# Optimization experiments

Measured on AMD Instinct MI355X. Metric: run time of the kernel, lower is better.

The kernel has to match this reference:

```python
import jax, jax.numpy as jnp
import numpy as np

FIX_SIGMA = (1.0, 2.0, 4.0, 8.0, 16.0)


def setup_inputs() -> dict:
    key = jax.random.key(0)
    k1, k2 = jax.random.split(key)
    B, C, D = 512, 32, 512
    source = jax.random.normal(k1, (B, C, D), dtype=jnp.float32)
    target = jax.random.normal(k2, (B, C, D), dtype=jnp.float32)
    return {"source": source, "target": target}


def _mmd(source, target):
    B = source.shape[0]
    total = jnp.concatenate([source, target], axis=0)  # [N, C, D], N = 2B
    # Pairwise per-channel squared L2 distance via norm expansion
    # (mathematically identical to ((x_i - x_j)**2).sum(-1), no [N,N,C,D] intermediate)
    sq = jnp.sum(total * total, axis=-1)  # [N, C]
    cross = jnp.einsum("icd,jcd->ijc", total, total)  # [N, N, C]
    L2 = sq[:, None, :] + sq[None, :, :] - 2.0 * cross  # [N, N, C]
    kernels = sum(jnp.exp(-L2 / sigma) for sigma in FIX_SIGMA)  # [N, N, C]
    XX = kernels[:B, :B, :]
    YY = kernels[B:, B:, :]
    XY = kernels[:B, B:, :]
    YX = kernels[B:, :B, :]
    loss_1 = XX + YY - XY - YX  # [B, B, C]
    # mean over dim0, mean over dim0 again (i.e. both batch dims), sum over channels
    return jnp.sum(jnp.mean(loss_1, axis=(0, 1)))


def reference(source, target):
    return _mmd(source, target)
```

## Files before the change

kernel.cpp:

```cpp
#include <hip/hip_runtime.h>

namespace {

constexpr int kC = 32;
constexpr int kD = 512;
constexpr int kB = 512;
constexpr int kN = 1024;
constexpr int kCD = kC * kD;
constexpr int BM = 128;
constexpr int BK = 64;
constexpr int KSTEPS = kD / BK;
constexpr int TILES = kN / BM;
constexpr int NPAIRS = TILES * (TILES + 1) / 2;

typedef float f32x4 __attribute__((ext_vector_type(4)));
typedef short s16x8 __attribute__((ext_vector_type(8)));

__device__ inline unsigned int pack_bf16(float a, float b) {
  unsigned int ua = __float_as_uint(a);
  unsigned int ub = __float_as_uint(b);
  ua += 0x7fffu + ((ua >> 16) & 1u);
  ub += 0x7fffu + ((ub >> 16) & 1u);
  return (ua >> 16) | (ub & 0xffff0000u);
}

__global__ void prep_kernel(const float* __restrict__ src,
                            const float* __restrict__ tgt,
                            float* __restrict__ sq,
                            unsigned int* __restrict__ tot) {
  int gw = (blockIdx.x * blockDim.x + threadIdx.x) >> 6;
  int lane = threadIdx.x & 63;
  int i = gw >> 5;
  int c = gw & 31;
  const float* p = (i < kB ? src + (size_t)i * kCD
                           : tgt + (size_t)(i - kB) * kCD) + c * kD;
  f32x4 v0 = *(const f32x4*)(p + lane * 8);
  f32x4 v1 = *(const f32x4*)(p + lane * 8 + 4);

  uint4 w = make_uint4(pack_bf16(v0.x, v0.y), pack_bf16(v0.z, v0.w),
                       pack_bf16(v1.x, v1.y), pack_bf16(v1.z, v1.w));
  *(uint4*)(tot + (size_t)(c * kN + i) * (kD / 2) + lane * 4) = w;

  float s = v0.x * v0.x + v0.y * v0.y + v0.z * v0.z + v0.w * v0.w
          + v1.x * v1.x + v1.y * v1.y + v1.z * v1.z + v1.w * v1.w;
#pragma unroll
  for (int o = 32; o > 0; o >>= 1) s += __shfl_down(s, o);
  if (lane == 0) sq[c * kN + i] = s;
}

__launch_bounds__(256, 2)
__global__ void mmd_kernel(const unsigned short* __restrict__ tot,
                           const float* __restrict__ sq,
                           float* __restrict__ out) {
  int b = blockIdx.x;
  int c = b & 31;
  int p = b >> 5;
  int ti = 0;
  while (p >= TILES - ti) { p -= TILES - ti; ++ti; }
  int tj = ti + p;

  __shared__ __align__(16) unsigned short lA[2][BM * BK];
  __shared__ __align__(16) unsigned short lB[2][BM * BK];
  __shared__ float wsum[4];

  const int t = threadIdx.x;
  const int lane = t & 63;
  const int wid = t >> 6;
  const int wr = wid >> 1;
  const int wc = wid & 1;

  const unsigned short* gA = tot + (size_t)(c * kN + ti * BM) * kD;
  const unsigned short* gB = tot + (size_t)(c * kN + tj * BM) * kD;

  const int srow = lane >> 3;
  const int sslot = lane & 7;

  auto STAGE = [&](int buf, int ks) {
#pragma unroll
    for (int q = 0; q < 4; ++q) {
      int row = (q * 4 + wid) * 8 + srow;
      int chunk = sslot ^ (row & 7);
      const unsigned short* sa = gA + (size_t)row * kD + ks * BK + chunk * 8;
      const unsigned short* sb = gB + (size_t)row * kD + ks * BK + chunk * 8;
      __builtin_amdgcn_global_load_lds(
          (const __attribute__((address_space(1))) unsigned int*)sa,
          (__attribute__((address_space(3))) unsigned int*)&lA[buf][(q * 4 + wid) * 512],
          16, 0, 0);
      __builtin_amdgcn_global_load_lds(
          (const __attribute__((address_space(1))) unsigned int*)sb,
          (__attribute__((address_space(3))) unsigned int*)&lB[buf][(q * 4 + wid) * 512],
          16, 0, 0);
    }
  };

  f32x4 acc[4][4] = {};

  STAGE(0, 0);
  __syncthreads();

  int cur = 0;
  for (int ks = 0; ks < KSTEPS; ++ks) {
    if (ks + 1 < KSTEPS) STAGE(cur ^ 1, ks + 1);

    const s16x8* A8 = (const s16x8*)lA[cur];
    const s16x8* B8 = (const s16x8*)lB[cur];
#pragma unroll
    for (int kk = 0; kk < 2; ++kk) {
      s16x8 aF[4], bF[4];
#pragma unroll
      for (int m = 0; m < 4; ++m) {
        int row = wr * 64 + m * 16 + (lane & 15);
        aF[m] = A8[row * 8 + ((kk * 4 + (lane >> 4)) ^ (row & 7))];
      }
#pragma unroll
      for (int n = 0; n < 4; ++n) {
        int row = wc * 64 + n * 16 + (lane & 15);
        bF[n] = B8[row * 8 + ((kk * 4 + (lane >> 4)) ^ (row & 7))];
      }
#pragma unroll
      for (int m = 0; m < 4; ++m)
#pragma unroll
        for (int n = 0; n < 4; ++n)
          acc[m][n] = __builtin_amdgcn_mfma_f32_16x16x32_bf16(
              aF[m], bF[n], acc[m][n], 0, 0, 0);
    }

    __syncthreads();
    cur ^= 1;
  }

  const float sA = (ti < TILES / 2) ? 1.f : -1.f;
  const float sB = (tj < TILES / 2) ? 1.f : -1.f;
  const float scale = sA * sB * ((ti == tj) ? 1.f : 2.f) / 262144.f;
  const float* sqA = sq + c * kN + ti * BM;
  const float* sqB = sq + c * kN + tj * BM;

  float local = 0.f;
#pragma unroll
  for (int m = 0; m < 4; ++m) {
    float sqa_r[4];
#pragma unroll
    for (int rI = 0; rI < 4; ++rI)
      sqa_r[rI] = sqA[wr * 64 + m * 16 + (lane >> 4) * 4 + rI];
#pragma unroll
    for (int n = 0; n < 4; ++n) {
      float sqb_ = sqB[wc * 64 + n * 16 + (lane & 15)];
#pragma unroll
      for (int rI = 0; rI < 4; ++rI) {
        float L2 = sqa_r[rI] + sqb_ - 2.f * acc[m][n][rI];
        float tt = __expf(L2 * -0.0625f);
        float t2 = tt * tt, t4 = t2 * t2, t8 = t4 * t4;
        local += tt + t2 + t4 + t8 + t8 * t8;
      }
    }
  }

#pragma unroll
  for (int o = 32; o > 0; o >>= 1) local += __shfl_down(local, o);
  if (lane == 0) wsum[wid] = local;
  __syncthreads();
  if (t == 0)
    atomicAdd(out, (wsum[0] + wsum[1] + wsum[2] + wsum[3]) * scale);
}

}

extern "C" void kernel_launch(void* const* d_in, const int* in_sizes, int n_in,
                              void* d_out, int out_size, void* d_ws,
                              size_t ws_size, hipStream_t stream) {
  const float* src = (const float*)d_in[0];
  const float* tgt = (const float*)d_in[1];
  float* out = (float*)d_out;

  float* sq = (float*)d_ws;
  unsigned int* tot = (unsigned int*)((char*)d_ws + (size_t)kC * kN * 4);

  (void)hipMemsetAsync(d_out, 0, sizeof(float), stream);

  {
    int blocks = (kN * kC) / 4;
    prep_kernel<<<blocks, 256, 0, stream>>>(src, tgt, sq, tot);
  }
  {
    mmd_kernel<<<NPAIRS * kC, 256, 0, stream>>>((const unsigned short*)tot, sq, out);
  }
}
```

Measured before the change: 59.92 us.

## Halve K tile, new LDS swizzle layout, raise occupancy, fold memset into prep

Shrinks the K-step tile from 64 to 32, which halves LDS use per block, and raises the launch bound to 4 waves-per-SIMD occupancy. It replaces the row-XOR swizzle with a new paired-row layout and precomputed per-lane LDS offsets, so fragment reads need one pointer plus constant offsets. The output zeroing moves from a separate memset into the prep kernel, removing one launch. The cost is twice as many k-steps and barriers, plus a tighter register budget that could cause spills.

```diff
diff --git a/kernel.cpp b/kernel.cpp
--- a/kernel.cpp
+++ b/kernel.cpp
@@ -8,7 +8,7 @@
 constexpr int kN = 1024;
 constexpr int kCD = kC * kD;
 constexpr int BM = 128;
-constexpr int BK = 64;
+constexpr int BK = 32;
 constexpr int KSTEPS = kD / BK;
 constexpr int TILES = kN / BM;
 constexpr int NPAIRS = TILES * (TILES + 1) / 2;
@@ -27,7 +27,9 @@
 __global__ void prep_kernel(const float* __restrict__ src,
                             const float* __restrict__ tgt,
                             float* __restrict__ sq,
-                            unsigned int* __restrict__ tot) {
+                            unsigned int* __restrict__ tot,
+                            float* __restrict__ out) {
+  if (blockIdx.x == 0 && threadIdx.x == 0) *out = 0.f;
   int gw = (blockIdx.x * blockDim.x + threadIdx.x) >> 6;
   int lane = threadIdx.x & 63;
   int i = gw >> 5;
@@ -48,7 +50,7 @@
   if (lane == 0) sq[c * kN + i] = s;
 }
 
-__launch_bounds__(256, 2)
+__launch_bounds__(256, 4)
 __global__ void mmd_kernel(const unsigned short* __restrict__ tot,
                            const float* __restrict__ sq,
                            float* __restrict__ out) {
@@ -72,26 +74,31 @@
   const unsigned short* gA = tot + (size_t)(c * kN + ti * BM) * kD;
   const unsigned short* gB = tot + (size_t)(c * kN + tj * BM) * kD;
 
-  const int srow = lane >> 3;
-  const int sslot = lane & 7;
+  const int srow = ((lane >> 3) << 1) + ((lane >> 2) & 1);
+  const int scch = (lane & 3) ^ ((lane >> 3) & 3);
 
   auto STAGE = [&](int buf, int ks) {
 #pragma unroll
-    for (int q = 0; q < 4; ++q) {
-      int row = (q * 4 + wid) * 8 + srow;
-      int chunk = sslot ^ (row & 7);
-      const unsigned short* sa = gA + (size_t)row * kD + ks * BK + chunk * 8;
-      const unsigned short* sb = gB + (size_t)row * kD + ks * BK + chunk * 8;
+    for (int q = 0; q < 2; ++q) {
+      int i = wid * 2 + q;
+      int r = 16 * i + srow;
+      const unsigned short* sa = gA + (size_t)r * kD + ks * BK + scch * 8;
+      const unsigned short* sb = gB + (size_t)r * kD + ks * BK + scch * 8;
       __builtin_amdgcn_global_load_lds(
           (const __attribute__((address_space(1))) unsigned int*)sa,
-          (__attribute__((address_space(3))) unsigned int*)&lA[buf][(q * 4 + wid) * 512],
+          (__attribute__((address_space(3))) unsigned int*)&lA[buf][i * 512],
           16, 0, 0);
       __builtin_amdgcn_global_load_lds(
           (const __attribute__((address_space(1))) unsigned int*)sb,
-          (__attribute__((address_space(3))) unsigned int*)&lB[buf][(q * 4 + wid) * 512],
+          (__attribute__((address_space(3))) unsigned int*)&lB[buf][i * 512],
           16, 0, 0);
     }
   };
+
+  const int l15 = lane & 15;
+  const int s4 = lane >> 4;
+  const int laneoff = ((l15 >> 1) << 7) + ((l15 & 1) << 6) +
+                      ((s4 ^ ((l15 >> 1) & 3)) << 4);
 
   f32x4 acc[4][4] = {};
 
@@ -102,28 +109,19 @@
   for (int ks = 0; ks < KSTEPS; ++ks) {
     if (ks + 1 < KSTEPS) STAGE(cur ^ 1, ks + 1);
 
-    const s16x8* A8 = (const s16x8*)lA[cur];
-    const s16x8* B8 = (const s16x8*)lB[cur];
+    const char* Abase = (const char*)lA[cur] + wr * 4096 + laneoff;
+    const char* Bbase = (const char*)lB[cur] + wc * 4096 + laneoff;
+    s16x8 aF[4], bF[4];
 #pragma unroll
-    for (int kk = 0; kk < 2; ++kk) {
-      s16x8 aF[4], bF[4];
+    for (int m = 0; m < 4; ++m) aF[m] = *(const s16x8*)(Abase + m * 1024);
 #pragma unroll
-      for (int m = 0; m < 4; ++m) {
-        int row = wr * 64 + m * 16 + (lane & 15);
-        aF[m] = A8[row * 8 + ((kk * 4 + (lane >> 4)) ^ (row & 7))];
-      }
+    for (int n = 0; n < 4; ++n) bF[n] = *(const s16x8*)(Bbase + n * 1024);
 #pragma unroll
-      for (int n = 0; n < 4; ++n) {
-        int row = wc * 64 + n * 16 + (lane & 15);
-        bF[n] = B8[row * 8 + ((kk * 4 + (lane >> 4)) ^ (row & 7))];
-      }
+    for (int m = 0; m < 4; ++m)
 #pragma unroll
-      for (int m = 0; m < 4; ++m)
-#pragma unroll
-        for (int n = 0; n < 4; ++n)
-          acc[m][n] = __builtin_amdgcn_mfma_f32_16x16x32_bf16(
-              aF[m], bF[n], acc[m][n], 0, 0, 0);
-    }
+      for (int n = 0; n < 4; ++n)
+        acc[m][n] = __builtin_amdgcn_mfma_f32_16x16x32_bf16(
+            aF[m], bF[n], acc[m][n], 0, 0, 0);
 
     __syncthreads();
     cur ^= 1;
@@ -175,11 +173,9 @@
   float* sq = (float*)d_ws;
   unsigned int* tot = (unsigned int*)((char*)d_ws + (size_t)kC * kN * 4);
 
-  (void)hipMemsetAsync(d_out, 0, sizeof(float), stream);
-
   {
     int blocks = (kN * kC) / 4;
-    prep_kernel<<<blocks, 256, 0, stream>>>(src, tgt, sq, tot);
+    prep_kernel<<<blocks, 256, 0, stream>>>(src, tgt, sq, tot, out);
   }
   {
     mmd_kernel<<<NPAIRS * kC, 256, 0, stream>>>((const unsigned short*)tot, sq, out);
```

Result: faster. 53.80 us (-10.2%).
